# Kernel tuning notes

Hardware: AMD Instinct MI355X
Metric: run time of the kernel (lower is better)

## Reference

```python
import jax, jax.numpy as jnp
import numpy as np

TAU = 0.95
MARGIN = 1.0
NUM_NEG = 1

B, S = 4096, 4096
N_RERANK = 8192


def setup_inputs() -> dict:
    key = jax.random.key(0)
    k1, k2, k3 = jax.random.split(key, 3)
    rerank_y = jax.random.normal(k1, (N_RERANK, 1), dtype=jnp.float32)
    # probabilities in (0,1]; keep away from 0 since the loss takes log
    cut_y = jax.random.uniform(k2, (B, S, 1), dtype=jnp.float32, minval=1e-4, maxval=1.0)
    rerank_label = jnp.ones((B, 1), dtype=jnp.float32)  # unused (overwritten by ones in source)
    cut_label = jax.random.randint(k3, (B, S), 0, 2, dtype=jnp.int32)
    return {"rerank_y": rerank_y, "cut_y": cut_y, "rerank_label": rerank_label, "cut_label": cut_label}


def _f1_weights(cut_label):
    # Vectorized Metric_for_Loss.f1(labels[i], j): F1 at cut depth j+1.
    lab = cut_label.astype(jnp.float32)                      # [B,S]
    cum = jnp.cumsum(lab, axis=1)                            # relevant docs within top j+1
    k = jnp.arange(1, lab.shape[1] + 1, dtype=jnp.float32)   # cut depth
    total = jnp.sum(lab, axis=1, keepdims=True)              # total relevant per list
    prec = cum / k
    rec = jnp.where(total > 0, cum / jnp.maximum(total, 1.0), 0.0)
    den = prec + rec
    return jnp.where(den > 0, 2.0 * prec * rec / den, 0.0)   # [B,S]


def _attncut_loss(cut_y, cut_label):
    out2d = jnp.squeeze(cut_y, axis=2)                       # [B,S]
    r = _f1_weights(cut_label)
    # Faithful to source: q = exp(r/tau) is summed into norm_factor, then q := 1/norm_factor
    norm = jnp.sum(jnp.exp(r / TAU), axis=1, keepdims=True)  # [B,1]
    q = 1.0 / norm
    loss_mat = jnp.log(out2d) * q
    return -jnp.sum(loss_mat) / out2d.shape[0]


def _rerank_loss(rerank_y):
    y_pos = rerank_y[:: NUM_NEG + 1, :]                      # [B,1]
    y_neg = rerank_y[1 :: NUM_NEG + 1, :]                    # [B,1] (num_neg=1 -> cat of one)
    y_neg = jnp.mean(y_neg, axis=-1, keepdims=True)
    # margin_ranking_loss with y=1, reduction='mean'
    return jnp.mean(jnp.maximum(0.0, -(y_pos - y_neg) + MARGIN))


def reference(rerank_y, cut_y, rerank_label, cut_label):
    return _attncut_loss(cut_y, cut_label) + _rerank_loss(rerank_y)
```

## Files before the change

### kernel.cpp

```cpp
#include <hip/hip_runtime.h>

#define NROWS 4096
#define NCOLS 4096
#define TAU 0.95f
#define MARGIN 1.0f

__global__ __launch_bounds__(256) void attncut_kernel(
    const float* __restrict__ cut_y, const int* __restrict__ cut_label,
    float* __restrict__ partials) {
  const int row = blockIdx.x;
  const int t = threadIdx.x;
  const int lane = t & 63;
  const int wid = t >> 6;

  const int4* lab4 = (const int4*)(cut_label + (size_t)row * NCOLS) + t * 4;
  const float4* yy4 = (const float4*)(cut_y + (size_t)row * NCOLS) + t * 4;

  const int4 L0 = lab4[0], L1 = lab4[1], L2 = lab4[2], L3 = lab4[3];
  const float4 Y0 = yy4[0], Y1 = yy4[1], Y2 = yy4[2], Y3 = yy4[3];

  const int lsum = L0.x + L0.y + L0.z + L0.w + L1.x + L1.y + L1.z + L1.w +
                   L2.x + L2.y + L2.z + L2.w + L3.x + L3.y + L3.z + L3.w;

  int x = lsum;
#pragma unroll
  for (int off = 1; off < 64; off <<= 1) {
    int v = __shfl_up(x, off, 64);
    if (lane >= off) x += v;
  }
  __shared__ int wsum[4];
  if (lane == 63) wsum[wid] = x;
  __syncthreads();
  int prev = 0;
#pragma unroll
  for (int w = 0; w < 4; ++w)
    if (w < wid) prev += wsum[w];
  const int Ttot = wsum[0] + wsum[1] + wsum[2] + wsum[3];
  int c = prev + x - lsum;

  const float Tf = (float)Ttot;
  const float kbase = (float)(t * 16);
  float norm_acc = 0.f, log_acc = 0.f;

#define STEP(LAB, YV, J)                                           \
  {                                                                \
    c += (LAB);                                                    \
    const float kk = kbase + (float)((J) + 1);                     \
    const float r =                                                \
        (c > 0) ? __fdividef(2.0f * (float)c, kk + Tf) : 0.0f;     \
    norm_acc += __expf(r * (1.0f / TAU));                          \
    log_acc += __logf(YV);                                         \
  }

  STEP(L0.x, Y0.x, 0)  STEP(L0.y, Y0.y, 1)  STEP(L0.z, Y0.z, 2)  STEP(L0.w, Y0.w, 3)
  STEP(L1.x, Y1.x, 4)  STEP(L1.y, Y1.y, 5)  STEP(L1.z, Y1.z, 6)  STEP(L1.w, Y1.w, 7)
  STEP(L2.x, Y2.x, 8)  STEP(L2.y, Y2.y, 9)  STEP(L2.z, Y2.z, 10) STEP(L2.w, Y2.w, 11)
  STEP(L3.x, Y3.x, 12) STEP(L3.y, Y3.y, 13) STEP(L3.z, Y3.z, 14) STEP(L3.w, Y3.w, 15)
#undef STEP

#pragma unroll
  for (int off = 32; off > 0; off >>= 1) {
    norm_acc += __shfl_down(norm_acc, off, 64);
    log_acc += __shfl_down(log_acc, off, 64);
  }
  __shared__ float nred[4], lred[4];
  if (lane == 0) {
    nred[wid] = norm_acc;
    lred[wid] = log_acc;
  }
  __syncthreads();
  if (t == 0) {
    const float norm = nred[0] + nred[1] + nred[2] + nred[3];
    const float ls = lred[0] + lred[1] + lred[2] + lred[3];
    partials[row] = -ls / (norm * (float)NROWS);
  }
}

__global__ __launch_bounds__(256) void finish_kernel(
    const float* __restrict__ partials, const float* __restrict__ rerank_y,
    float* __restrict__ out) {
  const int t = threadIdx.x;
  const int lane = t & 63, wid = t >> 6;

  float acc = 0.f;
  const float4* p4 = (const float4*)partials;
#pragma unroll
  for (int i = 0; i < 4; ++i) {
    float4 v = p4[t + 256 * i];
    acc += (v.x + v.y) + (v.z + v.w);
  }

  float racc = 0.f;
  const float4* y4 = (const float4*)rerank_y;
#pragma unroll
  for (int i = 0; i < 8; ++i) {
    float4 v = y4[t + 256 * i];
    racc += fmaxf(0.f, MARGIN - (v.x - v.y));
    racc += fmaxf(0.f, MARGIN - (v.z - v.w));
  }
  acc += racc * (1.0f / 4096.0f);

#pragma unroll
  for (int off = 32; off > 0; off >>= 1) acc += __shfl_down(acc, off, 64);
  __shared__ float ws[4];
  if (lane == 0) ws[wid] = acc;
  __syncthreads();
  if (t == 0) out[0] = (ws[0] + ws[1]) + (ws[2] + ws[3]);
}

extern "C" void kernel_launch(void* const* d_in, const int* in_sizes, int n_in,
                              void* d_out, int out_size, void* d_ws, size_t ws_size,
                              hipStream_t stream) {
  const float* rerank_y = (const float*)d_in[0];
  const float* cut_y = (const float*)d_in[1];
  const int* cut_label = (const int*)d_in[3];
  float* out = (float*)d_out;
  float* partials = (float*)d_ws;

  attncut_kernel<<<NROWS, 256, 0, stream>>>(cut_y, cut_label, partials);
  finish_kernel<<<1, 256, 0, stream>>>(partials, rerank_y, out);
}
```

Baseline: 151.0 us.

## Coalesce row loads, pack dual prefix scans, and batch log via products

Each thread now loads four strided float4/int4 chunks instead of four contiguous ones, so every wavefront load instruction covers consecutive addresses. The prefix sum now runs over four segment counts, packed two per 32-bit word into 16-bit halves, and the per-segment offsets are rebuilt from the packed totals. The log term is computed as one log2 of a product of four values, scaled by ln2 at the end, which cuts transcendental instructions by four. The product of four values in (1e-4,1) can get close to underflow, which is a small accuracy risk, and the packed scans double the shuffle count.

Measured after the change: 151.3 us. Within noise of the previous version (+0.2%).

```diff
diff --git a/kernel.cpp b/kernel.cpp
--- a/kernel.cpp
+++ b/kernel.cpp
@@ -4,6 +4,8 @@
 #define NCOLS 4096
 #define TAU 0.95f
 #define MARGIN 1.0f
+#define INV_TAU (1.0f / TAU)
+#define LN2F 0.69314718056f
 
 __global__ __launch_bounds__(256) void attncut_kernel(
     const float* __restrict__ cut_y, const int* __restrict__ cut_label,
@@ -13,66 +15,115 @@
   const int lane = t & 63;
   const int wid = t >> 6;
 
-  const int4* lab4 = (const int4*)(cut_label + (size_t)row * NCOLS) + t * 4;
-  const float4* yy4 = (const float4*)(cut_y + (size_t)row * NCOLS) + t * 4;
+  const int4* lab4 = (const int4*)(cut_label + (size_t)row * NCOLS);
+  const float4* yy4 = (const float4*)(cut_y + (size_t)row * NCOLS);
 
-  const int4 L0 = lab4[0], L1 = lab4[1], L2 = lab4[2], L3 = lab4[3];
-  const float4 Y0 = yy4[0], Y1 = yy4[1], Y2 = yy4[2], Y3 = yy4[3];
+  const int4 L0 = lab4[t];
+  const int4 L1 = lab4[t + 256];
+  const int4 L2 = lab4[t + 512];
+  const int4 L3 = lab4[t + 768];
+  const float4 Y0 = yy4[t];
+  const float4 Y1 = yy4[t + 256];
+  const float4 Y2 = yy4[t + 512];
+  const float4 Y3 = yy4[t + 768];
 
-  const int lsum = L0.x + L0.y + L0.z + L0.w + L1.x + L1.y + L1.z + L1.w +
-                   L2.x + L2.y + L2.z + L2.w + L3.x + L3.y + L3.z + L3.w;
+  const int s0 = L0.x + L0.y + L0.z + L0.w;
+  const int s1 = L1.x + L1.y + L1.z + L1.w;
+  const int s2 = L2.x + L2.y + L2.z + L2.w;
+  const int s3 = L3.x + L3.y + L3.z + L3.w;
 
-  int x = lsum;
+  unsigned int pa = (unsigned int)s0 | ((unsigned int)s1 << 16);
+  unsigned int pb = (unsigned int)s2 | ((unsigned int)s3 << 16);
+
+  unsigned int xa = pa, xb = pb;
 #pragma unroll
   for (int off = 1; off < 64; off <<= 1) {
-    int v = __shfl_up(x, off, 64);
-    if (lane >= off) x += v;
+    unsigned int va = __shfl_up(xa, off, 64);
+    unsigned int vb = __shfl_up(xb, off, 64);
+    if (lane >= off) {
+      xa += va;
+      xb += vb;
+    }
   }
-  __shared__ int wsum[4];
-  if (lane == 63) wsum[wid] = x;
+  __shared__ unsigned int wsA[4], wsB[4];
+  if (lane == 63) {
+    wsA[wid] = xa;
+    wsB[wid] = xb;
+  }
   __syncthreads();
-  int prev = 0;
+  unsigned int prevA = 0, prevB = 0;
 #pragma unroll
   for (int w = 0; w < 4; ++w)
-    if (w < wid) prev += wsum[w];
-  const int Ttot = wsum[0] + wsum[1] + wsum[2] + wsum[3];
-  int c = prev + x - lsum;
+    if (w < wid) {
+      prevA += wsA[w];
+      prevB += wsB[w];
+    }
+  const unsigned int totA = wsA[0] + wsA[1] + wsA[2] + wsA[3];
+  const unsigned int totB = wsB[0] + wsB[1] + wsB[2] + wsB[3];
 
-  const float Tf = (float)Ttot;
-  const float kbase = (float)(t * 16);
-  float norm_acc = 0.f, log_acc = 0.f;
+  const unsigned int exA = prevA + xa - pa;
+  const unsigned int exB = prevB + xb - pb;
 
-#define STEP(LAB, YV, J)                                           \
-  {                                                                \
-    c += (LAB);                                                    \
-    const float kk = kbase + (float)((J) + 1);                     \
-    const float r =                                                \
-        (c > 0) ? __fdividef(2.0f * (float)c, kk + Tf) : 0.0f;     \
-    norm_acc += __expf(r * (1.0f / TAU));                          \
-    log_acc += __logf(YV);                                         \
+  const int q0 = (int)(totA & 0xffffu), q1 = (int)(totA >> 16);
+  const int q2 = (int)(totB & 0xffffu), q3 = (int)(totB >> 16);
+  const float Tf = (float)(q0 + q1 + q2 + q3);
+
+  int c0 = (int)(exA & 0xffffu);
+  int c1 = q0 + (int)(exA >> 16);
+  int c2 = q0 + q1 + (int)(exB & 0xffffu);
+  int c3 = q0 + q1 + q2 + (int)(exB >> 16);
+
+  float na = 0.f;
+  float l2 = 0.f;
+
+#define QSTEP(cv, LV, YV, EBASE)                                              \
+  {                                                                           \
+    const float db = (float)(EBASE) + Tf;                                     \
+    cv += LV.x;                                                               \
+    {                                                                         \
+      float r = (cv > 0) ? __fdividef(2.0f * (float)cv, db + 1.0f) : 0.f;     \
+      na += __expf(r * INV_TAU);                                              \
+    }                                                                         \
+    cv += LV.y;                                                               \
+    {                                                                         \
+      float r = (cv > 0) ? __fdividef(2.0f * (float)cv, db + 2.0f) : 0.f;     \
+      na += __expf(r * INV_TAU);                                              \
+    }                                                                         \
+    cv += LV.z;                                                               \
+    {                                                                         \
+      float r = (cv > 0) ? __fdividef(2.0f * (float)cv, db + 3.0f) : 0.f;     \
+      na += __expf(r * INV_TAU);                                              \
+    }                                                                         \
+    cv += LV.w;                                                               \
+    {                                                                         \
+      float r = (cv > 0) ? __fdividef(2.0f * (float)cv, db + 4.0f) : 0.f;     \
+      na += __expf(r * INV_TAU);                                              \
+    }                                                                         \
+     \
+    l2 += __log2f(YV.x * YV.y * YV.z * YV.w);                                 \
   }
 
-  STEP(L0.x, Y0.x, 0)  STEP(L0.y, Y0.y, 1)  STEP(L0.z, Y0.z, 2)  STEP(L0.w, Y0.w, 3)
-  STEP(L1.x, Y1.x, 4)  STEP(L1.y, Y1.y, 5)  STEP(L1.z, Y1.z, 6)  STEP(L1.w, Y1.w, 7)
-  STEP(L2.x, Y2.x, 8)  STEP(L2.y, Y2.y, 9)  STEP(L2.z, Y2.z, 10) STEP(L2.w, Y2.w, 11)
-  STEP(L3.x, Y3.x, 12) STEP(L3.y, Y3.y, 13) STEP(L3.z, Y3.z, 14) STEP(L3.w, Y3.w, 15)
-#undef STEP
+  QSTEP(c0, L0, Y0, 4 * t)
+  QSTEP(c1, L1, Y1, 1024 + 4 * t)
+  QSTEP(c2, L2, Y2, 2048 + 4 * t)
+  QSTEP(c3, L3, Y3, 3072 + 4 * t)
+#undef QSTEP
 
 #pragma unroll
   for (int off = 32; off > 0; off >>= 1) {
-    norm_acc += __shfl_down(norm_acc, off, 64);
-    log_acc += __shfl_down(log_acc, off, 64);
+    na += __shfl_down(na, off, 64);
+    l2 += __shfl_down(l2, off, 64);
   }
   __shared__ float nred[4], lred[4];
   if (lane == 0) {
-    nred[wid] = norm_acc;
-    lred[wid] = log_acc;
+    nred[wid] = na;
+    lred[wid] = l2;
   }
   __syncthreads();
   if (t == 0) {
     const float norm = nred[0] + nred[1] + nred[2] + nred[3];
-    const float ls = lred[0] + lred[1] + lred[2] + lred[3];
-    partials[row] = -ls / (norm * (float)NROWS);
+    const float lnsum = (lred[0] + lred[1] + lred[2] + lred[3]) * LN2F;
+    partials[row] = -lnsum / (norm * (float)NROWS);
   }
 }
 
```

## Map one wavefront per row and pack labels into bitmasks

Applied to the files above, without the earlier changes.

Each 64-lane wavefront now processes a whole row, with four rows per block. This removes the LDS exchange and block-level syncs in favour of wave shuffles. Labels are packed into 64-bit masks and counted with popcount. The log terms are merged by taking log2 of products of four values, which cuts transcendental work but can lose precision or underflow on small probabilities. Each lane now handles 64 contiguous elements with strided loads, so coalescing per load instruction is worse.

Result: slower. 164.9 us (+9.2%).

```diff
diff --git a/kernel.cpp b/kernel.cpp
--- a/kernel.cpp
+++ b/kernel.cpp
@@ -4,75 +4,79 @@
 #define NCOLS 4096
 #define TAU 0.95f
 #define MARGIN 1.0f
+#define INV_TAU (1.0f / TAU)
+#define LN2F 0.69314718056f
 
-__global__ __launch_bounds__(256) void attncut_kernel(
+__global__ __launch_bounds__(256, 4) void attncut_kernel(
     const float* __restrict__ cut_y, const int* __restrict__ cut_label,
     float* __restrict__ partials) {
-  const int row = blockIdx.x;
   const int t = threadIdx.x;
   const int lane = t & 63;
   const int wid = t >> 6;
+  const int row = (blockIdx.x << 2) | wid;
 
-  const int4* lab4 = (const int4*)(cut_label + (size_t)row * NCOLS) + t * 4;
-  const float4* yy4 = (const float4*)(cut_y + (size_t)row * NCOLS) + t * 4;
+  const size_t rbase = (size_t)row * NCOLS;
+  const int4* lb = (const int4*)(cut_label + rbase) + lane * 16;
+  const float4* yb = (const float4*)(cut_y + rbase) + lane * 16;
 
-  const int4 L0 = lab4[0], L1 = lab4[1], L2 = lab4[2], L3 = lab4[3];
-  const float4 Y0 = yy4[0], Y1 = yy4[1], Y2 = yy4[2], Y3 = yy4[3];
+  unsigned int blo = 0u, bhi = 0u;
+#pragma unroll
+  for (int j = 0; j < 8; ++j) {
+    const int4 L = lb[j];
+    const unsigned int nib =
+        (unsigned int)(L.x | (L.y << 1) | (L.z << 2) | (L.w << 3));
+    blo |= nib << (4 * j);
+  }
+#pragma unroll
+  for (int j = 0; j < 8; ++j) {
+    const int4 L = lb[j + 8];
+    const unsigned int nib =
+        (unsigned int)(L.x | (L.y << 1) | (L.z << 2) | (L.w << 3));
+    bhi |= nib << (4 * j);
+  }
+  const int lsum = __popc(blo) + __popc(bhi);
 
-  const int lsum = L0.x + L0.y + L0.z + L0.w + L1.x + L1.y + L1.z + L1.w +
-                   L2.x + L2.y + L2.z + L2.w + L3.x + L3.y + L3.z + L3.w;
+  float l2 = 0.f;
+#pragma unroll
+  for (int j = 0; j < 16; ++j) {
+    const float4 v = yb[j];
+    l2 += __log2f((v.x * v.y) * (v.z * v.w));
+  }
 
   int x = lsum;
 #pragma unroll
   for (int off = 1; off < 64; off <<= 1) {
-    int v = __shfl_up(x, off, 64);
+    const int v = __shfl_up(x, off, 64);
     if (lane >= off) x += v;
   }
-  __shared__ int wsum[4];
-  if (lane == 63) wsum[wid] = x;
-  __syncthreads();
-  int prev = 0;
+  const int Ttot = __shfl(x, 63, 64);
+  const float Tf = (float)Ttot;
+  float cf = (float)(x - lsum);
+
+  const float kb = (float)(lane * 64) + Tf;
+  float na = 0.f;
 #pragma unroll
-  for (int w = 0; w < 4; ++w)
-    if (w < wid) prev += wsum[w];
-  const int Ttot = wsum[0] + wsum[1] + wsum[2] + wsum[3];
-  int c = prev + x - lsum;
-
-  const float Tf = (float)Ttot;
-  const float kbase = (float)(t * 16);
-  float norm_acc = 0.f, log_acc = 0.f;
-
-#define STEP(LAB, YV, J)                                           \
-  {                                                                \
-    c += (LAB);                                                    \
-    const float kk = kbase + (float)((J) + 1);                     \
-    const float r =                                                \
-        (c > 0) ? __fdividef(2.0f * (float)c, kk + Tf) : 0.0f;     \
-    norm_acc += __expf(r * (1.0f / TAU));                          \
-    log_acc += __logf(YV);                                         \
+  for (int j = 0; j < 32; ++j) {
+    cf += (float)((blo >> j) & 1u);
+    const float r =
+        (cf > 0.f) ? __fdividef(2.0f * cf, kb + (float)(j + 1)) : 0.f;
+    na += __expf(r * INV_TAU);
   }
-
-  STEP(L0.x, Y0.x, 0)  STEP(L0.y, Y0.y, 1)  STEP(L0.z, Y0.z, 2)  STEP(L0.w, Y0.w, 3)
-  STEP(L1.x, Y1.x, 4)  STEP(L1.y, Y1.y, 5)  STEP(L1.z, Y1.z, 6)  STEP(L1.w, Y1.w, 7)
-  STEP(L2.x, Y2.x, 8)  STEP(L2.y, Y2.y, 9)  STEP(L2.z, Y2.z, 10) STEP(L2.w, Y2.w, 11)
-  STEP(L3.x, Y3.x, 12) STEP(L3.y, Y3.y, 13) STEP(L3.z, Y3.z, 14) STEP(L3.w, Y3.w, 15)
-#undef STEP
+#pragma unroll
+  for (int j = 0; j < 32; ++j) {
+    cf += (float)((bhi >> j) & 1u);
+    const float r =
+        (cf > 0.f) ? __fdividef(2.0f * cf, kb + (float)(j + 33)) : 0.f;
+    na += __expf(r * INV_TAU);
+  }
 
 #pragma unroll
   for (int off = 32; off > 0; off >>= 1) {
-    norm_acc += __shfl_down(norm_acc, off, 64);
-    log_acc += __shfl_down(log_acc, off, 64);
+    na += __shfl_down(na, off, 64);
+    l2 += __shfl_down(l2, off, 64);
   }
-  __shared__ float nred[4], lred[4];
   if (lane == 0) {
-    nred[wid] = norm_acc;
-    lred[wid] = log_acc;
-  }
-  __syncthreads();
-  if (t == 0) {
-    const float norm = nred[0] + nred[1] + nred[2] + nred[3];
-    const float ls = lred[0] + lred[1] + lred[2] + lred[3];
-    partials[row] = -ls / (norm * (float)NROWS);
+    partials[row] = -(l2 * LN2F) / (na * (float)NROWS);
   }
 }
 
@@ -117,6 +121,6 @@
   float* out = (float*)d_out;
   float* partials = (float*)d_ws;
 
-  attncut_kernel<<<NROWS, 256, 0, stream>>>(cut_y, cut_label, partials);
+  attncut_kernel<<<NROWS / 4, 256, 0, stream>>>(cut_y, cut_label, partials);
   finish_kernel<<<1, 256, 0, stream>>>(partials, rerank_y, out);
 }
```
